# Performance work log

Measured on AMD Instinct MI355X. Metric: run time of the kernel, lower is better.

Reference implementation:

```python
import jax, jax.numpy as jnp
import numpy as np

MAX_RANGE = 100.0


def _conv3x3(x, w, b):
    # x: [B,C,H,W], w: [2,C,3,3], b: [2]
    y = jax.lax.conv_general_dilated(
        x, w, window_strides=(1, 1), padding='SAME',
        dimension_numbers=('NCHW', 'OIHW', 'NCHW'))
    return y + b[None, :, None, None]


def setup_inputs() -> dict:
    key = jax.random.key(0)
    k1, k2, k3 = jax.random.split(key, 3)
    B, C, H, W = 4, 64, 64, 64
    x = jax.random.normal(k1, (B, C, H, W), dtype=jnp.float32)
    conv_w = jax.random.normal(k2, (2, C, 3, 3), dtype=jnp.float32) * 0.05
    conv_b = jax.random.normal(k3, (2,), dtype=jnp.float32) * 0.05
    return {'x': x, 'conv_w': conv_w, 'conv_b': conv_b}


def reference(x, conv_w, conv_b):
    # alpha, beta: [B,1,H,W]
    ab = MAX_RANGE * jnp.tanh(_conv3x3(x, conv_w, conv_b))
    alpha, beta = ab[:, 0:1], ab[:, 1:2]

    # Pairwise differences d[b,i,j,h,w] = beta[b]*x[b,i] - x[b,j]  -> [B,C,C,H,W]
    d = beta[:, :, None] * x[:, :, None] - x[:, None, :]
    a = alpha[:, :, None]  # [B,1,1,H,W]

    # softAbs: softmax over the pair {d, -d} weighted by clamped alpha*d logits
    v1 = jnp.clip(d * a, -MAX_RANGE, MAX_RANGE)
    v2 = jnp.clip(-d * a, -MAX_RANGE, MAX_RANGE)
    m = jnp.maximum(v1, v2)
    e1 = jnp.exp(v1 - m)
    e2 = jnp.exp(v2 - m)
    p1 = e1 / (e1 + e2)
    sabs = d * (2.0 * p1 - 1.0)  # d*p1 + (-d)*(1-p1)

    # mean over i (the expand dim) -> [B,C,H,W]
    tmp = jnp.mean(sabs, axis=1)

    # softArgMin over channel dim
    sam = jax.nn.softmax(jnp.clip(-tmp * alpha, -MAX_RANGE, MAX_RANGE), axis=1)

    # soft median, keepdims -> [B,1,H,W]
    return jnp.sum(x * sam, axis=1, keepdims=True)
```

## Files before the change

### kernel.cpp

```cpp
#include <hip/hip_runtime.h>
#include <math.h>

#define MAXR 100.0f

__global__ __launch_bounds__(256) void dsf_fused(const float* __restrict__ x,
                                                 const float* __restrict__ wg,
                                                 const float* __restrict__ bias,
                                                 float* __restrict__ out) {
    __shared__ float xs[64 * 3 * 18];
    __shared__ float xst[16 * 68];

    const int tid  = threadIdx.x;
    const int lane = tid & 63;
    const int wave = tid >> 6;

    const int p0 = blockIdx.x * 16;
    const int b  = p0 >> 12;
    const int h  = (p0 >> 6) & 63;
    const int w0 = p0 & 63;

    float w0r[9], w1r[9];
    #pragma unroll
    for (int k = 0; k < 9; ++k) {
        w0r[k] = wg[lane * 9 + k];
        w1r[k] = wg[576 + lane * 9 + k];
    }
    const float b0 = bias[0], b1 = bias[1];

    const float* xbase = x + b * 262144;
    for (int e = tid; e < 3456; e += 256) {
        int c   = e / 54;
        int rem = e - c * 54;
        int r   = rem / 18;
        int wt  = rem - r * 18;
        int hh  = h + r - 1;
        int ww  = w0 - 1 + wt;
        float v = 0.f;
        if (hh >= 0 && hh < 64 && ww >= 0 && ww < 64)
            v = xbase[c * 4096 + hh * 64 + ww];
        xs[e] = v;
        if (r == 1 && wt >= 1 && wt <= 16) xst[(wt - 1) * 68 + c] = v;
    }
    __syncthreads();

    const float* xsl = xs + lane * 54;

    for (int k = 0; k < 4; ++k) {
        const int wl = wave * 4 + k;
        const int p  = p0 + wl;

        float a0 = 0.f, a1 = 0.f;
        #pragma unroll
        for (int r = 0; r < 3; ++r) {
            #pragma unroll
            for (int t = 0; t < 3; ++t) {
                float xv = xsl[r * 18 + wl + t];
                a0 = fmaf(xv, w0r[r * 3 + t], a0);
                a1 = fmaf(xv, w1r[r * 3 + t], a1);
            }
        }
        #pragma unroll
        for (int off = 32; off; off >>= 1) {
            a0 += __shfl_xor(a0, off, 64);
            a1 += __shfl_xor(a1, off, 64);
        }
        const float al = MAXR * tanhf(a0 + b0);
        const float be = MAXR * tanhf(a1 + b1);
        const float aa = fabsf(al);
        const float n2aa = -2.0f * aa;

        const float* xr = xst + wl * 68;
        const float xj = xr[lane];

        float A = 0.0f;
        #pragma unroll
        for (int ii = 0; ii < 64; ii += 4) {
            float4 xi4 = *(const float4*)(xr + ii);
            #pragma unroll
            for (int u = 0; u < 4; ++u) {
                float xi = (u == 0) ? xi4.x : (u == 1) ? xi4.y : (u == 2) ? xi4.z : xi4.w;
                float dd = fmaf(be, xi, -xj);
                float ad = fabsf(dd);
                float e2 = __expf(n2aa * ad);
                float t  = (1.0f - e2) * __builtin_amdgcn_rcpf(1.0f + e2);
                A = fmaf(ad, t, A);
            }
        }

        float gl = fmaxf(-A * aa * (1.0f / 64.0f), -MAXR);

        float gm = gl;
        #pragma unroll
        for (int off = 32; off; off >>= 1) gm = fmaxf(gm, __shfl_xor(gm, off, 64));
        float ew  = __expf(gl - gm);
        float den = ew, num = xj * ew;
        #pragma unroll
        for (int off = 32; off; off >>= 1) {
            den += __shfl_xor(den, off, 64);
            num += __shfl_xor(num, off, 64);
        }
        if (lane == 0) out[p] = num / den;
    }
}

extern "C" void kernel_launch(void* const* d_in, const int* in_sizes, int n_in,
                              void* d_out, int out_size, void* d_ws, size_t ws_size,
                              hipStream_t stream) {
    const float* x      = (const float*)d_in[0];
    const float* conv_w = (const float*)d_in[1];
    const float* conv_b = (const float*)d_in[2];
    float* out = (float*)d_out;
    (void)d_ws; (void)ws_size;

    dsf_fused<<<1024, 256, 0, stream>>>(x, conv_w, conv_b, out);
}
```

Before: 88.25 us.

## Shrink per-block tile to four pixels and launch four times more blocks

Each block now handles 4 pixels (one per wave) instead of 16, so the grid grows from 1024 to 4096 blocks. Halo loading shrinks to a 6-wide strip, conv weights are staged in shared memory instead of registers, and tanhf is replaced by an exp/rcp approximation. The intent is more parallelism and occupancy across the GPU's compute units, plus a cheaper tanh. The cost is more redundant halo and weight loads per pixel, and a less exact tanh.

```diff
diff --git a/kernel.cpp b/kernel.cpp
--- a/kernel.cpp
+++ b/kernel.cpp
@@ -3,104 +3,98 @@
 
 #define MAXR 100.0f
 
-__global__ __launch_bounds__(256) void dsf_fused(const float* __restrict__ x,
-                                                 const float* __restrict__ wg,
-                                                 const float* __restrict__ bias,
-                                                 float* __restrict__ out) {
-    __shared__ float xs[64 * 3 * 18];
-    __shared__ float xst[16 * 68];
+__device__ __forceinline__ float tanh_fast(float s) {
+    float as = fabsf(s);
+    float e2 = __expf(-2.0f * as);
+    float t  = (1.0f - e2) * __builtin_amdgcn_rcpf(1.0f + e2);
+    return copysignf(t, s);
+}
+
+__global__ __launch_bounds__(256, 8) void dsf_fused(const float* __restrict__ x,
+                                                    const float* __restrict__ wg,
+                                                    const float* __restrict__ bias,
+                                                    float* __restrict__ out) {
+    __shared__ float xs[64 * 19];
+    __shared__ float wl[1152];
+    __shared__ float xst[4 * 68];
 
     const int tid  = threadIdx.x;
     const int lane = tid & 63;
     const int wave = tid >> 6;
 
-    const int p0 = blockIdx.x * 16;
+    const int p0 = blockIdx.x * 4;
     const int b  = p0 >> 12;
     const int h  = (p0 >> 6) & 63;
     const int w0 = p0 & 63;
 
-    float w0r[9], w1r[9];
-    #pragma unroll
-    for (int k = 0; k < 9; ++k) {
-        w0r[k] = wg[lane * 9 + k];
-        w1r[k] = wg[576 + lane * 9 + k];
-    }
-    const float b0 = bias[0], b1 = bias[1];
+    for (int e = tid; e < 1152; e += 256) wl[e] = wg[e];
 
     const float* xbase = x + b * 262144;
-    for (int e = tid; e < 3456; e += 256) {
-        int c   = e / 54;
-        int rem = e - c * 54;
-        int r   = rem / 18;
-        int wt  = rem - r * 18;
+    for (int e = tid; e < 1152; e += 256) {
+        int c   = e / 18;
+        int rem = e - c * 18;
+        int r   = rem / 6;
+        int wt  = rem - r * 6;
         int hh  = h + r - 1;
         int ww  = w0 - 1 + wt;
         float v = 0.f;
         if (hh >= 0 && hh < 64 && ww >= 0 && ww < 64)
             v = xbase[c * 4096 + hh * 64 + ww];
-        xs[e] = v;
-        if (r == 1 && wt >= 1 && wt <= 16) xst[(wt - 1) * 68 + c] = v;
+        xs[c * 19 + rem] = v;
+        if (r == 1 && wt >= 1 && wt <= 4) xst[(wt - 1) * 68 + c] = v;
     }
     __syncthreads();
 
-    const float* xsl = xs + lane * 54;
+    const int p = p0 + wave;
 
-    for (int k = 0; k < 4; ++k) {
-        const int wl = wave * 4 + k;
-        const int p  = p0 + wl;
+    const float* xc  = xs + lane * 19;
+    const float* wle = wl + lane * 9;
+    float a0 = 0.f, a1 = 0.f;
+    #pragma unroll
+    for (int r = 0; r < 3; ++r) {
+        #pragma unroll
+        for (int t = 0; t < 3; ++t) {
+            float xv = xc[r * 6 + wave + t];
+            a0 = fmaf(xv, wle[r * 3 + t], a0);
+            a1 = fmaf(xv, wle[576 + r * 3 + t], a1);
+        }
+    }
+    #pragma unroll
+    for (int off = 32; off; off >>= 1) {
+        a0 += __shfl_xor(a0, off, 64);
+        a1 += __shfl_xor(a1, off, 64);
+    }
+    const float al = MAXR * tanh_fast(a0 + bias[0]);
+    const float be = MAXR * tanh_fast(a1 + bias[1]);
+    const float aa = fabsf(al);
+    const float n2aa = -2.0f * aa;
 
-        float a0 = 0.f, a1 = 0.f;
-        #pragma unroll
-        for (int r = 0; r < 3; ++r) {
-            #pragma unroll
-            for (int t = 0; t < 3; ++t) {
-                float xv = xsl[r * 18 + wl + t];
-                a0 = fmaf(xv, w0r[r * 3 + t], a0);
-                a1 = fmaf(xv, w1r[r * 3 + t], a1);
-            }
-        }
-        #pragma unroll
-        for (int off = 32; off; off >>= 1) {
-            a0 += __shfl_xor(a0, off, 64);
-            a1 += __shfl_xor(a1, off, 64);
-        }
-        const float al = MAXR * tanhf(a0 + b0);
-        const float be = MAXR * tanhf(a1 + b1);
-        const float aa = fabsf(al);
-        const float n2aa = -2.0f * aa;
+    const float* xr = xst + wave * 68;
+    const float xj = xr[lane];
+    float A = 0.0f;
+    #pragma unroll 4
+    for (int i = 0; i < 64; ++i) {
+        float xi = xr[i];
+        float dd = fmaf(be, xi, -xj);
+        float ad = fabsf(dd);
+        float e2 = __expf(n2aa * ad);
+        float t  = (1.0f - e2) * __builtin_amdgcn_rcpf(1.0f + e2);
+        A = fmaf(ad, t, A);
+    }
 
-        const float* xr = xst + wl * 68;
-        const float xj = xr[lane];
+    float gl = fmaxf(-A * aa * (1.0f / 64.0f), -MAXR);
 
-        float A = 0.0f;
-        #pragma unroll
-        for (int ii = 0; ii < 64; ii += 4) {
-            float4 xi4 = *(const float4*)(xr + ii);
-            #pragma unroll
-            for (int u = 0; u < 4; ++u) {
-                float xi = (u == 0) ? xi4.x : (u == 1) ? xi4.y : (u == 2) ? xi4.z : xi4.w;
-                float dd = fmaf(be, xi, -xj);
-                float ad = fabsf(dd);
-                float e2 = __expf(n2aa * ad);
-                float t  = (1.0f - e2) * __builtin_amdgcn_rcpf(1.0f + e2);
-                A = fmaf(ad, t, A);
-            }
-        }
-
-        float gl = fmaxf(-A * aa * (1.0f / 64.0f), -MAXR);
-
-        float gm = gl;
-        #pragma unroll
-        for (int off = 32; off; off >>= 1) gm = fmaxf(gm, __shfl_xor(gm, off, 64));
-        float ew  = __expf(gl - gm);
-        float den = ew, num = xj * ew;
-        #pragma unroll
-        for (int off = 32; off; off >>= 1) {
-            den += __shfl_xor(den, off, 64);
-            num += __shfl_xor(num, off, 64);
-        }
-        if (lane == 0) out[p] = num / den;
+    float gm = gl;
+    #pragma unroll
+    for (int off = 32; off; off >>= 1) gm = fmaxf(gm, __shfl_xor(gm, off, 64));
+    float ew  = __expf(gl - gm);
+    float den = ew, num = xj * ew;
+    #pragma unroll
+    for (int off = 32; off; off >>= 1) {
+        den += __shfl_xor(den, off, 64);
+        num += __shfl_xor(num, off, 64);
     }
+    if (lane == 0) out[p] = num / den;
 }
 
 extern "C" void kernel_launch(void* const* d_in, const int* in_sizes, int n_in,
@@ -112,5 +106,5 @@
     float* out = (float*)d_out;
     (void)d_ws; (void)ws_size;
 
-    dsf_fused<<<1024, 256, 0, stream>>>(x, conv_w, conv_b, out);
+    dsf_fused<<<4096, 256, 0, stream>>>(x, conv_w, conv_b, out);
 }
```

After: 85.64 us. -3.0%, faster.
